# Performance work log

Hardware: AMD Instinct MI355X
Metric: run time of the kernel (lower is better)

The kernel has to match this reference:

```python
import jax, jax.numpy as jnp
import numpy as np

# Module hyper-params (from init_kwargs)
M = 41            # filter taps (odd)
OVERLAPS = 40     # even
STRIDES = 216
N_FFT = OVERLAPS + STRIDES   # 256
HOP = STRIDES                # strides > 0 -> hop = strides
PAD = M // 2


def setup_inputs() -> dict:
    key = jax.random.key(0)
    ks = jax.random.split(key, 5)
    B, Nmodes = 2, 2
    steps = 4628
    L = (steps - 1) * HOP + N_FFT  # 999688, frames tile the signal exactly
    x_real = jax.random.normal(ks[0], (B, L, Nmodes), jnp.float32)
    x_imag = jax.random.normal(ks[1], (B, L, Nmodes), jnp.float32)
    task_info = jax.random.uniform(ks[2], (B, 4), jnp.float32)  # col 0 = power (dBm)
    # SnseFilter learned complex taps (shared across polarizations, step=1, n_fwm=0)
    h_real = jax.random.normal(ks[3], (M,), jnp.float32) * 0.01
    h_imag = jax.random.normal(ks[4], (M,), jnp.float32) * 0.01
    return {"x_real": x_real, "x_imag": x_imag, "task_info": task_info,
            "h_real": h_real, "h_imag": h_imag}


def _corr1d(I, h):
    # I: [N, Lp] real, h: [M] real -> valid cross-correlation [N, Lp-M+1]
    out = jax.lax.conv_general_dilated(I[:, None, :], h.reshape(1, 1, M),
                                       window_strides=(1,), padding='VALID')
    return out[:, 0, :]


def reference(x_real, x_imag, task_info, h_real, h_imag):
    x = x_real + 1j * x_imag          # [B, L, Nmodes] complex64
    B, L, Nm = x.shape
    steps = (L - N_FFT) // HOP + 1

    # ---- STFT along dim=1 (frame + FFT, rectangular window, center=False) ----
    idx = HOP * jnp.arange(steps)[:, None] + jnp.arange(N_FFT)[None, :]  # [steps, n_fft]
    frames = x[:, idx, :]                      # [B, steps, n_fft, Nm]
    X = jnp.fft.fft(frames, axis=2)            # frequency-domain frames

    # ---- periodic padding along frequency axis + SnseFilter (per-tap nonlinear PBC) ----
    Xp = jnp.concatenate([X[:, :, -PAD:, :], X, X[:, :, :PAD, :]], axis=2)  # [B,steps,Lp,Nm]
    I = jnp.sum(Xp.real ** 2 + Xp.imag ** 2, axis=-1)   # total intensity over modes [B,steps,Lp]
    Lp = N_FFT + 2 * PAD
    Ic = I.reshape(B * steps, Lp)
    phi = (_corr1d(Ic, h_real) + 1j * _corr1d(Ic, h_imag)).reshape(B, steps, N_FFT)
    # launch power from task_info (col 0 in dBm), per mode
    P = (10.0 ** (task_info[:, 0] / 10.0) / Nm).astype(jnp.float32)  # [B]
    # first-order perturbation: E_out = E + j * P * (h * I) * E  (Manakov diagonal term)
    Y = X * (1.0 + 1j * P[:, None, None, None] * phi[..., None])

    # ---- ISTFT: ifft each frame + overlap-add with rectangular-window normalization ----
    yf = jnp.fft.ifft(Y, axis=2)               # [B, steps, n_fft, Nm]
    flat_idx = idx.reshape(-1)
    ola = jnp.zeros((B, L, Nm), yf.dtype).at[:, flat_idx, :].add(
        yf.reshape(B, steps * N_FFT, Nm))
    wsum = jnp.zeros((L,), jnp.float32).at[flat_idx].add(1.0)  # frame coverage count
    y = ola / wsum[None, :, None]

    out = y[:, OVERLAPS // 2: L - OVERLAPS // 2, :]   # [B, L-overlaps, Nm] complex
    return jnp.stack([out.real, out.imag], axis=-1)    # real view [B, L-overlaps, Nm, 2]
```

## Files before the change

kernel.cpp:

```cpp
#include <hip/hip_runtime.h>
#include <hip/hip_fp16.h>
#include <math.h>

constexpr int NFFT = 256;
constexpr int HOP  = 216;
constexpr int PAD  = 20;

constexpr int CBS = 264;
constexpr int IPB = 544;
constexpr int IPS = 336;
constexpr int SMF = IPB + 2 * IPS;

__device__ __forceinline__ void cmul(float& dr, float& di, float ar, float ai, float br, float bi) {
    dr = ar * br - ai * bi;
    di = ar * bi + ai * br;
}

constexpr float TC16[10] = {1.f, 0.92387953f, 0.70710678f, 0.38268343f, 0.f,
                            -0.38268343f, -0.70710678f, -0.92387953f, -1.f, -0.92387953f};
constexpr float TS16[10] = {0.f, 0.38268343f, 0.70710678f, 0.92387953f, 1.f,
                            0.92387953f, 0.70710678f, 0.38268343f, 0.f, -0.38268343f};

template<int SGN>
__device__ __forceinline__ void fft16(float xr[16], float xi[16]) {
    constexpr float S = (float)SGN;
    float tr[4][4], ti[4][4];
    #pragma unroll
    for (int n1 = 0; n1 < 4; ++n1) {
        float ar = xr[n1],      ai = xi[n1];
        float br = xr[n1 + 4],  bi = xi[n1 + 4];
        float cr = xr[n1 + 8],  ci = xi[n1 + 8];
        float dr = xr[n1 + 12], di = xi[n1 + 12];
        float Ar = ar + cr, Ai = ai + ci, Br = ar - cr, Bi = ai - ci;
        float Cr = br + dr, Ci = bi + di, Dr = br - dr, Di = bi - di;
        tr[n1][0] = Ar + Cr;      ti[n1][0] = Ai + Ci;
        tr[n1][2] = Ar - Cr;      ti[n1][2] = Ai - Ci;
        tr[n1][1] = Br - S * Di;  ti[n1][1] = Bi + S * Dr;
        tr[n1][3] = Br + S * Di;  ti[n1][3] = Bi - S * Dr;
    }
    #pragma unroll
    for (int n1 = 1; n1 < 4; ++n1) {
        #pragma unroll
        for (int k2 = 1; k2 < 4; ++k2) {
            const int m = n1 * k2;
            const float wr = TC16[m], wi = S * TS16[m];
            float vr, vi;
            cmul(vr, vi, tr[n1][k2], ti[n1][k2], wr, wi);
            tr[n1][k2] = vr; ti[n1][k2] = vi;
        }
    }
    #pragma unroll
    for (int k2 = 0; k2 < 4; ++k2) {
        float ar = tr[0][k2], ai = ti[0][k2];
        float br = tr[1][k2], bi = ti[1][k2];
        float cr = tr[2][k2], ci = ti[2][k2];
        float dr = tr[3][k2], di = ti[3][k2];
        float Ar = ar + cr, Ai = ai + ci, Br = ar - cr, Bi = ai - ci;
        float Cr = br + dr, Ci = bi + di, Dr = br - dr, Di = bi - di;
        xr[k2]      = Ar + Cr;     xi[k2]      = Ai + Ci;
        xr[k2 + 8]  = Ar - Cr;     xi[k2 + 8]  = Ai - Ci;
        xr[k2 + 4]  = Br - S * Di; xi[k2 + 4]  = Bi + S * Dr;
        xr[k2 + 12] = Br + S * Di; xi[k2 + 12] = Bi - S * Dr;
    }
}

__device__ __forceinline__ void twiddle_seq(float xr[16], float xi[16], float wr0, float wi0) {
    float wkr = wr0, wki = wi0;
    #pragma unroll
    for (int k = 1; k < 16; ++k) {
        float vr, vi;
        cmul(vr, vi, xr[k], xi[k], wkr, wki);
        xr[k] = vr; xi[k] = vi;
        if (k < 15) {
            float nr, ni;
            cmul(nr, ni, wkr, wki, wr0, wi0);
            wkr = nr; wki = ni;
        }
    }
}

__global__ __launch_bounds__(256)
void zero_overlap(float4* __restrict__ out4, int B, int steps, int Lout) {
    const int total = B * (steps - 1) * 40;
    for (int idx = blockIdx.x * 256 + threadIdx.x; idx < total; idx += gridDim.x * 256) {
        const int j  = idx / 40;
        const int r4 = idx - j * 40;
        const int b  = j / (steps - 1);
        const int s  = j - b * (steps - 1) + 1;
        out4[(size_t)b * Lout + (size_t)s * HOP - PAD + r4] = make_float4(0.f, 0.f, 0.f, 0.f);
    }
}

__global__ __launch_bounds__(64)
void eq_pbc_kernel(const float* __restrict__ x_real,
                   const float* __restrict__ x_imag,
                   const float* __restrict__ task_info,
                   const float* __restrict__ h_real,
                   const float* __restrict__ h_imag,
                   float* __restrict__ out,
                   int B, int L, int steps)
{
    __shared__ __align__(16) float SM[SMF];

    const int tid = threadIdx.x;
    const int i   = tid & 15;
    const int fm  = tid >> 4;
    const int fr  = fm >> 1;
    const int md  = fm & 1;

    const int G = B * steps;
    int g = blockIdx.x * 2 + fr;
    const bool valid = (g < G);
    if (!valid) g = G - 1;
    const int b  = g / steps;
    const int s  = g - b * steps;
    const int l0 = s * HOP;

    float sb, cb;
    __sincosf(-6.2831853071795864f * (1.0f / 256.0f) * (float)i, &sb, &cb);

    float xr[16], xi[16];
    {
        const size_t base = ((size_t)b * L + l0) * 2 + (size_t)(2 * i + md);
        #pragma unroll
        for (int n2 = 0; n2 < 16; ++n2) {
            xr[n2] = x_real[base + 32 * n2];
            xi[n2] = x_imag[base + 32 * n2];
        }
    }

    fft16<-1>(xr, xi);
    twiddle_seq(xr, xi, cb, sb);

    const int tb = fm * 272;
    #pragma unroll
    for (int k = 0; k < 16; ++k) SM[tb + i * 17 + k] = xr[k];
    __syncthreads();
    #pragma unroll
    for (int n1 = 0; n1 < 16; ++n1) xr[n1] = SM[tb + n1 * 17 + i];
    __syncthreads();
    #pragma unroll
    for (int k = 0; k < 16; ++k) SM[tb + i * 17 + k] = xi[k];
    __syncthreads();
    #pragma unroll
    for (int n1 = 0; n1 < 16; ++n1) xi[n1] = SM[tb + n1 * 17 + i];

    fft16<-1>(xr, xi);
    __syncthreads();

    {
        float* ipf = &SM[IPB + fr * IPS];
        #pragma unroll
        for (int k1 = 0; k1 < 16; ++k1) {
            float v = xr[k1] * xr[k1] + xi[k1] * xi[k1];
            v += __shfl_xor(v, 16);
            if (!md && k1 < 8) {
                const int f = i + 16 * k1, p = f + PAD;
                ipf[p + (p >> 3)] = v;
                if (f < PAD) { const int p2 = f + 276; ipf[p2 + (p2 >> 3)] = v; }
            }
            if (md && k1 >= 8) {
                const int f = i + 16 * k1, p = f + PAD;
                ipf[p + (p >> 3)] = v;
                if (f >= 236) { const int p3 = f - 236; ipf[p3 + (p3 >> 3)] = v; }
            }
        }
    }
    __syncthreads();

    {
        const int u   = tid & 31;
        const int frq = tid >> 5;
        int g2 = blockIdx.x * 2 + frq;
        if (g2 >= G) g2 = G - 1;
        const int b2 = g2 / steps;
        const float* ipb = &SM[IPB + frq * IPS + 9 * u];
        float win[8];
        #pragma unroll
        for (int j = 0; j < 8; ++j) win[j] = ipb[j + (j >> 3)];
        float phr[8], phq[8];
        #pragma unroll
        for (int o = 0; o < 8; ++o) { phr[o] = 0.f; phq[o] = 0.f; }
        #pragma unroll
        for (int t = 0; t < 41; ++t) {
            const float htr = h_real[t], hti = h_imag[t];
            #pragma unroll
            for (int o = 0; o < 8; ++o) {
                const float wv = win[(t + o) & 7];
                phr[o] = fmaf(wv, htr, phr[o]);
                phq[o] = fmaf(wv, hti, phq[o]);
            }
            if (t < 40) { const int j = t + 8; win[t & 7] = ipb[j + (j >> 3)]; }
        }
        const float P = exp2f(task_info[4 * b2] * 0.33219280948873623f) * 0.5f;
        unsigned* C = (unsigned*)SM;
        #pragma unroll
        for (int o = 0; o < 8; ++o) {
            __half2 h2 = __floats2half2_rn(1.0f - P * phq[o], P * phr[o]);
            C[frq * CBS + 8 * u + o] = *(unsigned*)&h2;
        }
    }
    __syncthreads();

    {
        const unsigned* C = (const unsigned*)SM;
        #pragma unroll
        for (int k1 = 0; k1 < 16; ++k1) {
            const unsigned cu = C[fr * CBS + i + 16 * k1];
            const __half2 h2 = *(const __half2*)&cu;
            const float cr_ = __low2float(h2);
            const float ci_ = __high2float(h2);
            const float vr = xr[k1] * cr_ - xi[k1] * ci_;
            const float vi = xr[k1] * ci_ + xi[k1] * cr_;
            xr[k1] = vr; xi[k1] = vi;
        }
    }

    fft16<1>(xr, xi);
    twiddle_seq(xr, xi, cb, -sb);
    __syncthreads();

    #pragma unroll
    for (int k = 0; k < 16; ++k) SM[tb + i * 17 + k] = xr[k];
    __syncthreads();
    #pragma unroll
    for (int k2 = 0; k2 < 16; ++k2) xr[k2] = SM[tb + k2 * 17 + i];
    __syncthreads();
    #pragma unroll
    for (int k = 0; k < 16; ++k) SM[tb + i * 17 + k] = xi[k];
    __syncthreads();
    #pragma unroll
    for (int k2 = 0; k2 < 16; ++k2) xi[k2] = SM[tb + k2 * 17 + i];

    fft16<1>(xr, xi);

    if (valid) {
        const int Lout = L - 2 * PAD;
        float* obase = out + (size_t)b * Lout * 4 + md * 2;
        #pragma unroll
        for (int n2 = 0; n2 < 16; ++n2) {
            const int n  = i + 16 * n2;
            const int la = l0 + n;
            if (la < PAD || la >= L - PAD) continue;
            const bool ov = (n < NFFT - HOP && s > 0) || (n >= HOP && s + 1 < steps);
            const float sc = (ov ? 0.5f : 1.0f) * (1.0f / 256.0f);
            float* p = obase + (size_t)(la - PAD) * 4;
            const float vr = xr[n2] * sc, vi = xi[n2] * sc;
            if (ov) { atomicAdd(p, vr); atomicAdd(p + 1, vi); }
            else    { *(float2*)p = make_float2(vr, vi); }
        }
    }
}

extern "C" void kernel_launch(void* const* d_in, const int* in_sizes, int n_in,
                              void* d_out, int out_size, void* d_ws, size_t ws_size,
                              hipStream_t stream) {
    const float* x_real    = (const float*)d_in[0];
    const float* x_imag    = (const float*)d_in[1];
    const float* task_info = (const float*)d_in[2];
    const float* h_real    = (const float*)d_in[3];
    const float* h_imag    = (const float*)d_in[4];

    const int B     = in_sizes[2] / 4;
    const int L     = in_sizes[0] / (B * 2);
    const int steps = (L - NFFT) / HOP + 1;
    const int G     = B * steps;
    const int Lout  = L - 2 * PAD;

    if (steps > 1) {
        const int total4 = B * (steps - 1) * 40;
        const int zb = (total4 + 255) / 256;
        zero_overlap<<<zb, 256, 0, stream>>>((float4*)d_out, B, steps, Lout);
    }

    eq_pbc_kernel<<<(G + 1) / 2, 64, 0, stream>>>(
        x_real, x_imag, task_info, h_real, h_imag, (float*)d_out, B, L, steps);
}
```

Before: 116.7 us.

## Vectorize FFT with packed float2 math and single-pass complex LDS transposes

Rewrites the radix-16 FFT stages, twiddles and filter correlation to use two-wide float vectors, so the compiler can emit packed FP32 instructions. The shared-memory transpose now moves interleaved complex values in one pass with 128-bit stores, which removes the separate real and imaginary passes and several barriers. Filter taps are staged once in shared memory as duplicated pairs instead of being read from global memory inside the unrolled loop. The phase-correction coefficients are stored as fp32 instead of packed half, which uses more shared memory per block but avoids the precision loss of fp16.

```diff
diff --git a/kernel.cpp b/kernel.cpp
--- a/kernel.cpp
+++ b/kernel.cpp
@@ -6,14 +6,21 @@
 constexpr int HOP  = 216;
 constexpr int PAD  = 20;
 
-constexpr int CBS = 264;
-constexpr int IPB = 544;
-constexpr int IPS = 336;
-constexpr int SMF = IPB + 2 * IPS;
-
-__device__ __forceinline__ void cmul(float& dr, float& di, float ar, float ai, float br, float bi) {
-    dr = ar * br - ai * bi;
-    di = ar * bi + ai * br;
+typedef float v2f __attribute__((ext_vector_type(2)));
+
+constexpr int RS    = 18;
+constexpr int PLF   = 288;
+constexpr int CFS   = 288;
+constexpr int IPB_F = 1152;
+constexpr int IPS_F = 336;
+constexpr int HRB   = 1152;
+constexpr int HIB   = 1193;
+constexpr int SMV   = 1234;
+
+__device__ __forceinline__ v2f mkv2(float a, float b) { v2f r; r.x = a; r.y = b; return r; }
+
+__device__ __forceinline__ v2f cmul2(v2f a, v2f b) {
+    return a.xx * b + a.yy * mkv2(-b.y, b.x);
 }
 
 constexpr float TC16[10] = {1.f, 0.92387953f, 0.70710678f, 0.38268343f, 0.f,
@@ -22,61 +29,62 @@
                             0.92387953f, 0.70710678f, 0.38268343f, 0.f, -0.38268343f};
 
 template<int SGN>
-__device__ __forceinline__ void fft16(float xr[16], float xi[16]) {
-    constexpr float S = (float)SGN;
-    float tr[4][4], ti[4][4];
+__device__ __forceinline__ void fft16v(v2f x[16]) {
+    v2f t[4][4];
     #pragma unroll
     for (int n1 = 0; n1 < 4; ++n1) {
-        float ar = xr[n1],      ai = xi[n1];
-        float br = xr[n1 + 4],  bi = xi[n1 + 4];
-        float cr = xr[n1 + 8],  ci = xi[n1 + 8];
-        float dr = xr[n1 + 12], di = xi[n1 + 12];
-        float Ar = ar + cr, Ai = ai + ci, Br = ar - cr, Bi = ai - ci;
-        float Cr = br + dr, Ci = bi + di, Dr = br - dr, Di = bi - di;
-        tr[n1][0] = Ar + Cr;      ti[n1][0] = Ai + Ci;
-        tr[n1][2] = Ar - Cr;      ti[n1][2] = Ai - Ci;
-        tr[n1][1] = Br - S * Di;  ti[n1][1] = Bi + S * Dr;
-        tr[n1][3] = Br + S * Di;  ti[n1][3] = Bi - S * Dr;
+        v2f a = x[n1], b = x[n1 + 4], c = x[n1 + 8], d = x[n1 + 12];
+        v2f A = a + c, B = a - c, C = b + d, D = b - d;
+        v2f jD = mkv2(-D.y, D.x);
+        t[n1][0] = A + C;
+        t[n1][2] = A - C;
+        if (SGN < 0) { t[n1][1] = B - jD; t[n1][3] = B + jD; }
+        else         { t[n1][1] = B + jD; t[n1][3] = B - jD; }
     }
     #pragma unroll
     for (int n1 = 1; n1 < 4; ++n1) {
         #pragma unroll
         for (int k2 = 1; k2 < 4; ++k2) {
             const int m = n1 * k2;
-            const float wr = TC16[m], wi = S * TS16[m];
-            float vr, vi;
-            cmul(vr, vi, tr[n1][k2], ti[n1][k2], wr, wi);
-            tr[n1][k2] = vr; ti[n1][k2] = vi;
+            const float wr = TC16[m], wi = (float)SGN * TS16[m];
+            v2f v = t[n1][k2];
+            t[n1][k2] = wr * v + wi * mkv2(-v.y, v.x);
         }
     }
     #pragma unroll
     for (int k2 = 0; k2 < 4; ++k2) {
-        float ar = tr[0][k2], ai = ti[0][k2];
-        float br = tr[1][k2], bi = ti[1][k2];
-        float cr = tr[2][k2], ci = ti[2][k2];
-        float dr = tr[3][k2], di = ti[3][k2];
-        float Ar = ar + cr, Ai = ai + ci, Br = ar - cr, Bi = ai - ci;
-        float Cr = br + dr, Ci = bi + di, Dr = br - dr, Di = bi - di;
-        xr[k2]      = Ar + Cr;     xi[k2]      = Ai + Ci;
-        xr[k2 + 8]  = Ar - Cr;     xi[k2 + 8]  = Ai - Ci;
-        xr[k2 + 4]  = Br - S * Di; xi[k2 + 4]  = Bi + S * Dr;
-        xr[k2 + 12] = Br + S * Di; xi[k2 + 12] = Bi - S * Dr;
-    }
-}
-
-__device__ __forceinline__ void twiddle_seq(float xr[16], float xi[16], float wr0, float wi0) {
-    float wkr = wr0, wki = wi0;
-    #pragma unroll
-    for (int k = 1; k < 16; ++k) {
-        float vr, vi;
-        cmul(vr, vi, xr[k], xi[k], wkr, wki);
-        xr[k] = vr; xi[k] = vi;
-        if (k < 15) {
-            float nr, ni;
-            cmul(nr, ni, wkr, wki, wr0, wi0);
-            wkr = nr; wki = ni;
-        }
-    }
+        v2f a = t[0][k2], b = t[1][k2], c = t[2][k2], d = t[3][k2];
+        v2f A = a + c, B = a - c, C = b + d, D = b - d;
+        v2f jD = mkv2(-D.y, D.x);
+        x[k2]      = A + C;
+        x[k2 + 8]  = A - C;
+        if (SGN < 0) { x[k2 + 4] = B - jD; x[k2 + 12] = B + jD; }
+        else         { x[k2 + 4] = B + jD; x[k2 + 12] = B - jD; }
+    }
+}
+
+__device__ __forceinline__ void twiddle4(v2f x[16], v2f w1) {
+    const v2f w2 = cmul2(w1, w1);
+    const v2f w4 = cmul2(w2, w2);
+    const v2f w8 = cmul2(w4, w4);
+    x[1] = cmul2(x[1], w1);
+    x[2] = cmul2(x[2], w2);
+    x[3] = cmul2(x[3], cmul2(w2, w1));
+    v2f wk = w4;
+    x[4] = cmul2(x[4], wk);
+    wk = cmul2(wk, w1); x[5] = cmul2(x[5], wk);
+    wk = cmul2(wk, w1); x[6] = cmul2(x[6], wk);
+    wk = cmul2(wk, w1); x[7] = cmul2(x[7], wk);
+    v2f wm = w8;
+    x[8] = cmul2(x[8], wm);
+    wm = cmul2(wm, w1); x[9]  = cmul2(x[9],  wm);
+    wm = cmul2(wm, w1); x[10] = cmul2(x[10], wm);
+    wm = cmul2(wm, w1); x[11] = cmul2(x[11], wm);
+    v2f wn = cmul2(w8, w4);
+    x[12] = cmul2(x[12], wn);
+    wn = cmul2(wn, w1); x[13] = cmul2(x[13], wn);
+    wn = cmul2(wn, w1); x[14] = cmul2(x[14], wn);
+    wn = cmul2(wn, w1); x[15] = cmul2(x[15], wn);
 }
 
 __global__ __launch_bounds__(256)
@@ -100,7 +108,8 @@
                    float* __restrict__ out,
                    int B, int L, int steps)
 {
-    __shared__ __align__(16) float SM[SMF];
+    __shared__ __align__(16) v2f SM2[SMV];
+    float* SMf = (float*)SM2;
 
     const int tid = threadIdx.x;
     const int i   = tid & 15;
@@ -116,43 +125,45 @@
     const int s  = g - b * steps;
     const int l0 = s * HOP;
 
+    if (tid < 41) {
+        const float hr = h_real[tid], hi = h_imag[tid];
+        SM2[HRB + tid] = mkv2(hr, hr);
+        SM2[HIB + tid] = mkv2(hi, hi);
+    }
+
     float sb, cb;
     __sincosf(-6.2831853071795864f * (1.0f / 256.0f) * (float)i, &sb, &cb);
 
-    float xr[16], xi[16];
+    v2f X[16];
     {
         const size_t base = ((size_t)b * L + l0) * 2 + (size_t)(2 * i + md);
         #pragma unroll
-        for (int n2 = 0; n2 < 16; ++n2) {
-            xr[n2] = x_real[base + 32 * n2];
-            xi[n2] = x_imag[base + 32 * n2];
-        }
-    }
-
-    fft16<-1>(xr, xi);
-    twiddle_seq(xr, xi, cb, sb);
-
-    const int tb = fm * 272;
-    #pragma unroll
-    for (int k = 0; k < 16; ++k) SM[tb + i * 17 + k] = xr[k];
-    __syncthreads();
-    #pragma unroll
-    for (int n1 = 0; n1 < 16; ++n1) xr[n1] = SM[tb + n1 * 17 + i];
-    __syncthreads();
-    #pragma unroll
-    for (int k = 0; k < 16; ++k) SM[tb + i * 17 + k] = xi[k];
-    __syncthreads();
-    #pragma unroll
-    for (int n1 = 0; n1 < 16; ++n1) xi[n1] = SM[tb + n1 * 17 + i];
-
-    fft16<-1>(xr, xi);
-    __syncthreads();
-
-    {
-        float* ipf = &SM[IPB + fr * IPS];
+        for (int n2 = 0; n2 < 16; ++n2)
+            X[n2] = mkv2(x_real[base + 32 * n2], x_imag[base + 32 * n2]);
+    }
+
+    fft16v<-1>(X);
+    twiddle4(X, mkv2(cb, sb));
+
+    const int tb2 = fm * PLF;
+    {
+        float4* rowp = (float4*)&SM2[tb2 + i * RS];
+        #pragma unroll
+        for (int k = 0; k < 16; k += 2)
+            rowp[k >> 1] = make_float4(X[k].x, X[k].y, X[k + 1].x, X[k + 1].y);
+    }
+    __syncthreads();
+    #pragma unroll
+    for (int n1 = 0; n1 < 16; ++n1) X[n1] = SM2[tb2 + n1 * RS + i];
+
+    fft16v<-1>(X);
+    __syncthreads();
+
+    {
+        float* ipf = SMf + IPB_F + fr * IPS_F;
         #pragma unroll
         for (int k1 = 0; k1 < 16; ++k1) {
-            float v = xr[k1] * xr[k1] + xi[k1] * xi[k1];
+            float v = X[k1].x * X[k1].x + X[k1].y * X[k1].y;
             v += __shfl_xor(v, 16);
             if (!md && k1 < 8) {
                 const int f = i + 16 * k1, p = f + PAD;
@@ -174,65 +185,66 @@
         int g2 = blockIdx.x * 2 + frq;
         if (g2 >= G) g2 = G - 1;
         const int b2 = g2 / steps;
-        const float* ipb = &SM[IPB + frq * IPS + 9 * u];
-        float win[8];
-        #pragma unroll
-        for (int j = 0; j < 8; ++j) win[j] = ipb[j + (j >> 3)];
-        float phr[8], phq[8];
-        #pragma unroll
-        for (int o = 0; o < 8; ++o) { phr[o] = 0.f; phq[o] = 0.f; }
+        const float* ipb = SMf + IPB_F + frq * IPS_F + 9 * u;
+        float w_[9];
+        #pragma unroll
+        for (int j = 0; j < 9; ++j) w_[j] = ipb[j + (j >> 3)];
+        v2f W2[8];
+        #pragma unroll
+        for (int ss = 0; ss < 8; ++ss) W2[ss] = mkv2(w_[ss], w_[ss + 1]);
+        float carry = w_[8];
+        v2f pr[4], pq[4];
+        #pragma unroll
+        for (int m = 0; m < 4; ++m) { pr[m] = mkv2(0.f, 0.f); pq[m] = mkv2(0.f, 0.f); }
         #pragma unroll
         for (int t = 0; t < 41; ++t) {
-            const float htr = h_real[t], hti = h_imag[t];
+            const v2f h2r = SM2[HRB + t];
+            const v2f h2i = SM2[HIB + t];
             #pragma unroll
-            for (int o = 0; o < 8; ++o) {
-                const float wv = win[(t + o) & 7];
-                phr[o] = fmaf(wv, htr, phr[o]);
-                phq[o] = fmaf(wv, hti, phq[o]);
-            }
-            if (t < 40) { const int j = t + 8; win[t & 7] = ipb[j + (j >> 3)]; }
+            for (int m = 0; m < 4; ++m) {
+                const v2f wp = W2[(t + 2 * m) & 7];
+                pr[m] += wp * h2r;
+                pq[m] += wp * h2i;
+            }
+            if (t < 39) {
+                const int j = t + 9;
+                const float nw = ipb[j + (j >> 3)];
+                W2[(t + 8) & 7] = mkv2(carry, nw);
+                carry = nw;
+            }
         }
         const float P = exp2f(task_info[4 * b2] * 0.33219280948873623f) * 0.5f;
-        unsigned* C = (unsigned*)SM;
-        #pragma unroll
-        for (int o = 0; o < 8; ++o) {
-            __half2 h2 = __floats2half2_rn(1.0f - P * phq[o], P * phr[o]);
-            C[frq * CBS + 8 * u + o] = *(unsigned*)&h2;
-        }
-    }
-    __syncthreads();
-
-    {
-        const unsigned* C = (const unsigned*)SM;
+        float4* cp = (float4*)&SM2[frq * CFS + 8 * u + 2 * (u >> 1)];
+        #pragma unroll
+        for (int m = 0; m < 4; ++m)
+            cp[m] = make_float4(1.0f - P * pq[m].x, P * pr[m].x,
+                                1.0f - P * pq[m].y, P * pr[m].y);
+    }
+    __syncthreads();
+
+    {
         #pragma unroll
         for (int k1 = 0; k1 < 16; ++k1) {
-            const unsigned cu = C[fr * CBS + i + 16 * k1];
-            const __half2 h2 = *(const __half2*)&cu;
-            const float cr_ = __low2float(h2);
-            const float ci_ = __high2float(h2);
-            const float vr = xr[k1] * cr_ - xi[k1] * ci_;
-            const float vi = xr[k1] * ci_ + xi[k1] * cr_;
-            xr[k1] = vr; xi[k1] = vi;
-        }
-    }
-
-    fft16<1>(xr, xi);
-    twiddle_seq(xr, xi, cb, -sb);
-    __syncthreads();
-
-    #pragma unroll
-    for (int k = 0; k < 16; ++k) SM[tb + i * 17 + k] = xr[k];
-    __syncthreads();
-    #pragma unroll
-    for (int k2 = 0; k2 < 16; ++k2) xr[k2] = SM[tb + k2 * 17 + i];
-    __syncthreads();
-    #pragma unroll
-    for (int k = 0; k < 16; ++k) SM[tb + i * 17 + k] = xi[k];
-    __syncthreads();
-    #pragma unroll
-    for (int k2 = 0; k2 < 16; ++k2) xi[k2] = SM[tb + k2 * 17 + i];
-
-    fft16<1>(xr, xi);
+            const v2f c = SM2[fr * CFS + i + 18 * k1];
+            X[k1] = cmul2(X[k1], c);
+        }
+    }
+
+    fft16v<1>(X);
+    twiddle4(X, mkv2(cb, -sb));
+    __syncthreads();
+
+    {
+        float4* rowp = (float4*)&SM2[tb2 + i * RS];
+        #pragma unroll
+        for (int k = 0; k < 16; k += 2)
+            rowp[k >> 1] = make_float4(X[k].x, X[k].y, X[k + 1].x, X[k + 1].y);
+    }
+    __syncthreads();
+    #pragma unroll
+    for (int k2 = 0; k2 < 16; ++k2) X[k2] = SM2[tb2 + k2 * RS + i];
+
+    fft16v<1>(X);
 
     if (valid) {
         const int Lout = L - 2 * PAD;
@@ -245,7 +257,7 @@
             const bool ov = (n < NFFT - HOP && s > 0) || (n >= HOP && s + 1 < steps);
             const float sc = (ov ? 0.5f : 1.0f) * (1.0f / 256.0f);
             float* p = obase + (size_t)(la - PAD) * 4;
-            const float vr = xr[n2] * sc, vi = xi[n2] * sc;
+            const float vr = X[n2].x * sc, vi = X[n2].y * sc;
             if (ov) { atomicAdd(p, vr); atomicAdd(p + 1, vi); }
             else    { *(float2*)p = make_float2(vr, vi); }
         }
```

Result: no change. 115.3 us (-1.2%).
